# Optimization experiments

Hardware: AMD Instinct MI355X
Metric: run time of the kernel (lower is better)

Reference implementation:

```python
import jax, jax.numpy as jnp
import numpy as np

CELL_SIDE = 1.0
GRID_N = 6  # n x n occupancy grid


def _occupancy_grid(obs2):
    """Vectorized pairwise occupancy binning.
    obs2: [N, 2] -> grid [N, GRID_N*GRID_N] (counts of other pedestrians per cell)."""
    N = obs2.shape[0]
    nn = GRID_N * GRID_N
    # rel[i, j] = position of pedestrian j relative to i, in grid coords
    rel = (obs2[None, :, :] - obs2[:, None, :]) / CELL_SIDE + GRID_N / 2  # [N, N, 2]
    in_range = jnp.all((rel >= 0) & (rel < GRID_N), axis=-1)              # [N, N]
    not_self = ~jnp.eye(N, dtype=bool)
    valid = ~jnp.isnan(obs2[:, 0])                                        # [N]
    mask = in_range & not_self & valid[:, None] & valid[None, :]
    ij = jnp.clip(rel.astype(jnp.int32), 0, GRID_N - 1)                   # floor (rel>=0 under mask)
    local_bin = ij[..., 0] * GRID_N + ij[..., 1]                          # [N, N]
    # Global segment id: row i owns bins [i*nn, (i+1)*nn); invalid -> trash bin N*nn
    seg = jnp.where(mask, jnp.arange(N, dtype=jnp.int32)[:, None] * nn + local_bin, N * nn)
    counts = jax.ops.segment_sum(mask.astype(jnp.float32).reshape(-1),
                                 seg.reshape(-1), num_segments=N * nn + 1)
    return counts[: N * nn].reshape(N, nn)


def setup_inputs() -> dict:
    key = jax.random.key(0)
    k1, k2, k3, k4, k5 = jax.random.split(key, 5)
    N, hidden_dim, nn = 8192, 128, GRID_N * GRID_N
    hidden_state = jax.random.normal(k1, (N, hidden_dim), dtype=jnp.float32)
    obs1 = jax.random.normal(k2, (N, 2), dtype=jnp.float32)
    obs2 = jax.random.normal(k3, (N, 2), dtype=jnp.float32)
    W = jax.random.normal(k4, (hidden_dim, nn), dtype=jnp.float32) * (1.0 / np.sqrt(nn))
    b = jax.random.normal(k5, (hidden_dim,), dtype=jnp.float32) * 0.01
    return {"hidden_state": hidden_state, "obs1": obs1, "obs2": obs2, "W": W, "b": b}


def reference(hidden_state, obs1, obs2, W, b):
    # type_='occupancy': grid depends only on obs2; then Linear embedding.
    grid = _occupancy_grid(obs2)              # [N, 36]
    return grid @ W.T + b                     # [N, 128]
```

## Files before the change

### kernel.cpp

```cpp
#include <hip/hip_runtime.h>

#define N_PED  8192
#define HID    128
#define NN     36
#define IPB    8
#define SLICES 64
#define BLOCK  512
#define JS     128
#define HWW    10
#define NB     1024

__device__ __forceinline__ void rmw2(float p0x, float p0y, float p1x, float p1y,
                                     float xi4, float yi4, unsigned vone,
                                     unsigned baseA, unsigned baseB) {
    unsigned tA, iA, aA, vA, tB, iB, aB, vB;
    asm volatile(
        "v_sub_f32 %[tA], %[p0x], %[xi4]\n\t"
        "v_sub_f32 %[iA], %[p0y], %[yi4]\n\t"
        "v_sub_f32 %[tB], %[p1x], %[xi4]\n\t"
        "v_sub_f32 %[iB], %[p1y], %[yi4]\n\t"
        "v_cvt_i32_f32 %[tA], %[tA]\n\t"
        "v_cvt_i32_f32 %[iA], %[iA]\n\t"
        "v_cvt_i32_f32 %[tB], %[tB]\n\t"
        "v_cvt_i32_f32 %[iB], %[iB]\n\t"
        "v_add_u32 %[tA], -1, %[tA]\n\t"
        "v_add_u32 %[iA], -1, %[iA]\n\t"
        "v_add_u32 %[tB], -1, %[tB]\n\t"
        "v_add_u32 %[iB], -1, %[iB]\n\t"
        "v_max_u32 %[aA], %[tA], %[iA]\n\t"
        "v_max_u32 %[aB], %[tB], %[iB]\n\t"
        "v_mad_u32_u24 %[tA], %[tA], 6, %[iA]\n\t"
        "v_mad_u32_u24 %[tB], %[tB], 6, %[iB]\n\t"
        "v_cmp_gt_u32 vcc, 6, %[aA]\n\t"
        "v_lshrrev_b32 %[aA], 2, %[tA]\n\t"
        "v_cndmask_b32 %[aA], 9, %[aA], vcc\n\t"
        "v_cmp_gt_u32 vcc, 6, %[aB]\n\t"
        "v_lshrrev_b32 %[aB], 2, %[tB]\n\t"
        "v_cndmask_b32 %[aB], 9, %[aB], vcc\n\t"
        "v_lshlrev_b32 %[iA], 3, %[tA]\n\t"
        "v_lshlrev_b32 %[iA], %[iA], %[one]\n\t"
        "v_lshlrev_b32 %[iB], 3, %[tB]\n\t"
        "v_lshlrev_b32 %[iB], %[iB], %[one]\n\t"
        "v_lshl_add_u32 %[aA], %[aA], 11, %[bA]\n\t"
        "v_lshl_add_u32 %[aB], %[aB], 11, %[bB]\n\t"
        "ds_read_b32 %[vA], %[aA]\n\t"
        "ds_read_b32 %[vB], %[aB]\n\t"
        "s_waitcnt lgkmcnt(0)\n\t"
        "v_add_u32 %[vA], %[vA], %[iA]\n\t"
        "v_add_u32 %[vB], %[vB], %[iB]\n\t"
        "ds_write_b32 %[aA], %[vA]\n\t"
        "ds_write_b32 %[aB], %[vB]\n\t"
        : [tA]"=&v"(tA), [iA]"=&v"(iA), [aA]"=&v"(aA), [vA]"=&v"(vA),
          [tB]"=&v"(tB), [iB]"=&v"(iB), [aB]"=&v"(aB), [vB]"=&v"(vB)
        : [p0x]"v"(p0x), [p0y]"v"(p0y), [p1x]"v"(p1x), [p1y]"v"(p1y),
          [xi4]"v"(xi4), [yi4]"v"(yi4), [one]"v"(vone),
          [bA]"v"(baseA), [bB]"v"(baseB)
        : "vcc");
}

__global__ __launch_bounds__(BLOCK, 6) void pool_kernel(
    const float* __restrict__ obs2_g,
    const float* __restrict__ Wg,
    const float* __restrict__ bias,
    float* __restrict__ out)
{
    __shared__ unsigned s_hA[HWW * BLOCK];
    __shared__ unsigned s_hB[HWW * BLOCK];
    __shared__ float    s_rgrid[IPB][NN];
    __shared__ unsigned s_wsel[IPB];

    const int tid = threadIdx.x;
    const int bid = blockIdx.x;

    #pragma unroll
    for (int k = 0; k < HWW; ++k) {
        s_hA[tid + k * BLOCK] = 0u;
        s_hB[tid + k * BLOCK] = 0u;
    }

    const int il    = tid & (IPB - 1);
    const int slice = tid >> 3;
    const int i     = bid * IPB + il;

    const float2 pi = ((const float2*)obs2_g)[i];
    const float  xi4 = pi.x - 4.0f;
    const float  yi4 = pi.y - 4.0f;

    if (tid < IPB) {
        float dx = pi.x - xi4;
        float dy = pi.y - yi4;
        unsigned u1 = (unsigned)((int)dx) - 1u;
        unsigned u2 = (unsigned)((int)dy) - 1u;
        bool ok = (u1 < 6u) & (u2 < 6u);
        s_wsel[il] = ok ? (u1 * 6u + u2) : 255u;
    }
    __syncthreads();

    const unsigned vone  = 1u;
    const unsigned baseA = (unsigned)(uintptr_t)&s_hA[tid];
    const unsigned baseB = (unsigned)(uintptr_t)&s_hB[tid];

    #define PAIR8(r0, r1, r2, r3) do {                              \
        rmw2(r0.x, r0.y, r0.z, r0.w, xi4, yi4, vone, baseA, baseB); \
        rmw2(r1.x, r1.y, r1.z, r1.w, xi4, yi4, vone, baseA, baseB); \
        rmw2(r2.x, r2.y, r2.z, r2.w, xi4, yi4, vone, baseA, baseB); \
        rmw2(r3.x, r3.y, r3.z, r3.w, xi4, yi4, vone, baseA, baseB); \
    } while (0)

    {
        const float4* jp = (const float4*)obs2_g + slice * (JS / 2);
        float4 a0 = jp[0], a1 = jp[1], a2 = jp[2], a3 = jp[3];
        float4 b0 = jp[4], b1 = jp[5], b2 = jp[6], b3 = jp[7];
        jp += 8;
        #pragma unroll 1
        for (int it = 0; it < 7; ++it) {
            PAIR8(a0, a1, a2, a3);
            a0 = jp[0]; a1 = jp[1]; a2 = jp[2]; a3 = jp[3];
            PAIR8(b0, b1, b2, b3);
            b0 = jp[4]; b1 = jp[5]; b2 = jp[6]; b3 = jp[7];
            jp += 8;
        }
        PAIR8(a0, a1, a2, a3);
        PAIR8(b0, b1, b2, b3);
    }
    #undef PAIR8

    asm volatile("s_waitcnt lgkmcnt(0)" ::: "memory");
    __syncthreads();

    if (tid < IPB * 9) {
        const int ril = tid & (IPB - 1);
        const int w   = tid >> 3;
        unsigned lo = 0u, hi = 0u;
        #pragma unroll 8
        for (int sl = 0; sl < SLICES; ++sl) {
            unsigned t = sl * IPB + ril;
            unsigned a = s_hA[(w << 9) + t];
            unsigned b = s_hB[(w << 9) + t];
            lo += (a & 0x00FF00FFu) + (b & 0x00FF00FFu);
            hi += ((a >> 8) & 0x00FF00FFu) + ((b >> 8) & 0x00FF00FFu);
        }
        unsigned s0 = lo & 0xFFFFu;
        unsigned s1 = hi & 0xFFFFu;
        unsigned s2 = lo >> 16;
        unsigned s3 = hi >> 16;
        const unsigned sel  = s_wsel[ril];
        const unsigned base = (unsigned)(w * 4);
        s0 -= (sel == base + 0u);
        s1 -= (sel == base + 1u);
        s2 -= (sel == base + 2u);
        s3 -= (sel == base + 3u);
        s_rgrid[ril][base + 0] = (float)s0;
        s_rgrid[ril][base + 1] = (float)s1;
        s_rgrid[ril][base + 2] = (float)s2;
        s_rgrid[ril][base + 3] = (float)s3;
    }
    __syncthreads();

    const int h  = tid & (HID - 1);
    const int r0 = tid >> 7;
    const float4* W4 = (const float4*)Wg;

    const float bh = bias[h];
    float acc0 = bh, acc1 = bh;

    #pragma unroll
    for (int k4 = 0; k4 < 9; ++k4) {
        float4 w4 = W4[h * 9 + k4];
        float4 g0 = *(const float4*)&s_rgrid[r0    ][k4 * 4];
        float4 g1 = *(const float4*)&s_rgrid[r0 + 4][k4 * 4];
        acc0 += g0.x * w4.x + g0.y * w4.y + g0.z * w4.z + g0.w * w4.w;
        acc1 += g1.x * w4.x + g1.y * w4.y + g1.z * w4.z + g1.w * w4.w;
    }

    const int obase = bid * IPB;
    out[(obase + r0    ) * HID + h] = acc0;
    out[(obase + r0 + 4) * HID + h] = acc1;
}

extern "C" void kernel_launch(void* const* d_in, const int* in_sizes, int n_in,
                              void* d_out, int out_size, void* d_ws, size_t ws_size,
                              hipStream_t stream) {
    const float* obs2 = (const float*)d_in[2];
    const float* W    = (const float*)d_in[3];
    const float* b    = (const float*)d_in[4];
    float* out        = (float*)d_out;
    (void)in_sizes; (void)n_in; (void)out_size; (void)d_ws; (void)ws_size;

    hipLaunchKernelGGL(pool_kernel, dim3(NB), dim3(BLOCK), 0, stream,
                       obs2, W, b, out);
}
```

Baseline: 39.32 us.

## Halve block size, use four private LDS histogram copies with masked increments

```diff
diff --git a/kernel.cpp b/kernel.cpp
--- a/kernel.cpp
+++ b/kernel.cpp
@@ -4,16 +4,19 @@
 #define HID    128
 #define NN     36
 #define IPB    8
-#define SLICES 64
-#define BLOCK  512
-#define JS     128
-#define HWW    10
+#define SLICES 32
+#define BLOCK  256
+#define JS     256
 #define NB     1024
-
-__device__ __forceinline__ void rmw2(float p0x, float p0y, float p1x, float p1y,
-                                     float xi4, float yi4, unsigned vone,
-                                     unsigned baseA, unsigned baseB) {
-    unsigned tA, iA, aA, vA, tB, iB, aB, vB;
+#define AWORDS (9 * BLOCK)
+
+__device__ __forceinline__ void quad4(
+    float p0x, float p0y, float p1x, float p1y,
+    float p2x, float p2y, float p3x, float p3y,
+    float xi4, float yi4, unsigned vone,
+    unsigned bA, unsigned bB, unsigned bC, unsigned bD)
+{
+    unsigned tA, tB, iA, aA, vA, iB, aB, vB, iC, aC, vC, iD, aD, vD;
     asm volatile(
         "v_sub_f32 %[tA], %[p0x], %[xi4]\n\t"
         "v_sub_f32 %[iA], %[p0y], %[yi4]\n\t"
@@ -33,39 +36,80 @@
         "v_mad_u32_u24 %[tB], %[tB], 6, %[iB]\n\t"
         "v_cmp_gt_u32 vcc, 6, %[aA]\n\t"
         "v_lshrrev_b32 %[aA], 2, %[tA]\n\t"
-        "v_cndmask_b32 %[aA], 9, %[aA], vcc\n\t"
+        "v_cndmask_b32 %[aA], 0, %[aA], vcc\n\t"
+        "v_lshlrev_b32 %[iA], 3, %[tA]\n\t"
+        "v_lshlrev_b32 %[iA], %[iA], %[one]\n\t"
+        "v_cndmask_b32 %[iA], 0, %[iA], vcc\n\t"
+        "v_lshl_add_u32 %[aA], %[aA], 10, %[bA]\n\t"
         "v_cmp_gt_u32 vcc, 6, %[aB]\n\t"
         "v_lshrrev_b32 %[aB], 2, %[tB]\n\t"
-        "v_cndmask_b32 %[aB], 9, %[aB], vcc\n\t"
-        "v_lshlrev_b32 %[iA], 3, %[tA]\n\t"
-        "v_lshlrev_b32 %[iA], %[iA], %[one]\n\t"
+        "v_cndmask_b32 %[aB], 0, %[aB], vcc\n\t"
         "v_lshlrev_b32 %[iB], 3, %[tB]\n\t"
         "v_lshlrev_b32 %[iB], %[iB], %[one]\n\t"
-        "v_lshl_add_u32 %[aA], %[aA], 11, %[bA]\n\t"
-        "v_lshl_add_u32 %[aB], %[aB], 11, %[bB]\n\t"
+        "v_cndmask_b32 %[iB], 0, %[iB], vcc\n\t"
+        "v_lshl_add_u32 %[aB], %[aB], 10, %[bB]\n\t"
         "ds_read_b32 %[vA], %[aA]\n\t"
         "ds_read_b32 %[vB], %[aB]\n\t"
+        "v_sub_f32 %[tA], %[p2x], %[xi4]\n\t"
+        "v_sub_f32 %[iC], %[p2y], %[yi4]\n\t"
+        "v_sub_f32 %[tB], %[p3x], %[xi4]\n\t"
+        "v_sub_f32 %[iD], %[p3y], %[yi4]\n\t"
+        "v_cvt_i32_f32 %[tA], %[tA]\n\t"
+        "v_cvt_i32_f32 %[iC], %[iC]\n\t"
+        "v_cvt_i32_f32 %[tB], %[tB]\n\t"
+        "v_cvt_i32_f32 %[iD], %[iD]\n\t"
+        "v_add_u32 %[tA], -1, %[tA]\n\t"
+        "v_add_u32 %[iC], -1, %[iC]\n\t"
+        "v_add_u32 %[tB], -1, %[tB]\n\t"
+        "v_add_u32 %[iD], -1, %[iD]\n\t"
+        "v_max_u32 %[aC], %[tA], %[iC]\n\t"
+        "v_max_u32 %[aD], %[tB], %[iD]\n\t"
+        "v_mad_u32_u24 %[tA], %[tA], 6, %[iC]\n\t"
+        "v_mad_u32_u24 %[tB], %[tB], 6, %[iD]\n\t"
+        "v_cmp_gt_u32 vcc, 6, %[aC]\n\t"
+        "v_lshrrev_b32 %[aC], 2, %[tA]\n\t"
+        "v_cndmask_b32 %[aC], 0, %[aC], vcc\n\t"
+        "v_lshlrev_b32 %[iC], 3, %[tA]\n\t"
+        "v_lshlrev_b32 %[iC], %[iC], %[one]\n\t"
+        "v_cndmask_b32 %[iC], 0, %[iC], vcc\n\t"
+        "v_lshl_add_u32 %[aC], %[aC], 10, %[bC]\n\t"
+        "v_cmp_gt_u32 vcc, 6, %[aD]\n\t"
+        "v_lshrrev_b32 %[aD], 2, %[tB]\n\t"
+        "v_cndmask_b32 %[aD], 0, %[aD], vcc\n\t"
+        "v_lshlrev_b32 %[iD], 3, %[tB]\n\t"
+        "v_lshlrev_b32 %[iD], %[iD], %[one]\n\t"
+        "v_cndmask_b32 %[iD], 0, %[iD], vcc\n\t"
+        "v_lshl_add_u32 %[aD], %[aD], 10, %[bD]\n\t"
+        "ds_read_b32 %[vC], %[aC]\n\t"
+        "ds_read_b32 %[vD], %[aD]\n\t"
         "s_waitcnt lgkmcnt(0)\n\t"
         "v_add_u32 %[vA], %[vA], %[iA]\n\t"
         "v_add_u32 %[vB], %[vB], %[iB]\n\t"
+        "v_add_u32 %[vC], %[vC], %[iC]\n\t"
+        "v_add_u32 %[vD], %[vD], %[iD]\n\t"
         "ds_write_b32 %[aA], %[vA]\n\t"
         "ds_write_b32 %[aB], %[vB]\n\t"
-        : [tA]"=&v"(tA), [iA]"=&v"(iA), [aA]"=&v"(aA), [vA]"=&v"(vA),
-          [tB]"=&v"(tB), [iB]"=&v"(iB), [aB]"=&v"(aB), [vB]"=&v"(vB)
+        "ds_write_b32 %[aC], %[vC]\n\t"
+        "ds_write_b32 %[aD], %[vD]\n\t"
+        : [tA]"=&v"(tA), [tB]"=&v"(tB),
+          [iA]"=&v"(iA), [aA]"=&v"(aA), [vA]"=&v"(vA),
+          [iB]"=&v"(iB), [aB]"=&v"(aB), [vB]"=&v"(vB),
+          [iC]"=&v"(iC), [aC]"=&v"(aC), [vC]"=&v"(vC),
+          [iD]"=&v"(iD), [aD]"=&v"(aD), [vD]"=&v"(vD)
         : [p0x]"v"(p0x), [p0y]"v"(p0y), [p1x]"v"(p1x), [p1y]"v"(p1y),
+          [p2x]"v"(p2x), [p2y]"v"(p2y), [p3x]"v"(p3x), [p3y]"v"(p3y),
           [xi4]"v"(xi4), [yi4]"v"(yi4), [one]"v"(vone),
-          [bA]"v"(baseA), [bB]"v"(baseB)
+          [bA]"v"(bA), [bB]"v"(bB), [bC]"v"(bC), [bD]"v"(bD)
         : "vcc");
 }
 
-__global__ __launch_bounds__(BLOCK, 6) void pool_kernel(
+__global__ __launch_bounds__(BLOCK, 4) void pool_kernel(
     const float* __restrict__ obs2_g,
     const float* __restrict__ Wg,
     const float* __restrict__ bias,
     float* __restrict__ out)
 {
-    __shared__ unsigned s_hA[HWW * BLOCK];
-    __shared__ unsigned s_hB[HWW * BLOCK];
+    __shared__ unsigned s_h[4 * AWORDS];
     __shared__ float    s_rgrid[IPB][NN];
     __shared__ unsigned s_wsel[IPB];
 
@@ -73,10 +117,8 @@
     const int bid = blockIdx.x;
 
     #pragma unroll
-    for (int k = 0; k < HWW; ++k) {
-        s_hA[tid + k * BLOCK] = 0u;
-        s_hB[tid + k * BLOCK] = 0u;
-    }
+    for (int k = 0; k < 36; ++k)
+        s_h[tid + k * BLOCK] = 0u;
 
     const int il    = tid & (IPB - 1);
     const int slice = tid >> 3;
@@ -96,15 +138,17 @@
     }
     __syncthreads();
 
-    const unsigned vone  = 1u;
-    const unsigned baseA = (unsigned)(uintptr_t)&s_hA[tid];
-    const unsigned baseB = (unsigned)(uintptr_t)&s_hB[tid];
-
-    #define PAIR8(r0, r1, r2, r3) do {                              \
-        rmw2(r0.x, r0.y, r0.z, r0.w, xi4, yi4, vone, baseA, baseB); \
-        rmw2(r1.x, r1.y, r1.z, r1.w, xi4, yi4, vone, baseA, baseB); \
-        rmw2(r2.x, r2.y, r2.z, r2.w, xi4, yi4, vone, baseA, baseB); \
-        rmw2(r3.x, r3.y, r3.z, r3.w, xi4, yi4, vone, baseA, baseB); \
+    const unsigned vone = 1u;
+    const unsigned bA = (unsigned)(uintptr_t)&s_h[0 * AWORDS + tid];
+    const unsigned bB = (unsigned)(uintptr_t)&s_h[1 * AWORDS + tid];
+    const unsigned bC = (unsigned)(uintptr_t)&s_h[2 * AWORDS + tid];
+    const unsigned bD = (unsigned)(uintptr_t)&s_h[3 * AWORDS + tid];
+
+    #define PAIR8(r0, r1, r2, r3) do {                                   \
+        quad4(r0.x, r0.y, r0.z, r0.w, r1.x, r1.y, r1.z, r1.w,            \
+              xi4, yi4, vone, bA, bB, bC, bD);                           \
+        quad4(r2.x, r2.y, r2.z, r2.w, r3.x, r3.y, r3.z, r3.w,            \
+              xi4, yi4, vone, bA, bB, bC, bD);                           \
     } while (0)
 
     {
@@ -113,7 +157,7 @@
         float4 b0 = jp[4], b1 = jp[5], b2 = jp[6], b3 = jp[7];
         jp += 8;
         #pragma unroll 1
-        for (int it = 0; it < 7; ++it) {
+        for (int it = 0; it < 15; ++it) {
             PAIR8(a0, a1, a2, a3);
             a0 = jp[0]; a1 = jp[1]; a2 = jp[2]; a3 = jp[3];
             PAIR8(b0, b1, b2, b3);
@@ -132,13 +176,17 @@
         const int ril = tid & (IPB - 1);
         const int w   = tid >> 3;
         unsigned lo = 0u, hi = 0u;
-        #pragma unroll 8
+        #pragma unroll 4
         for (int sl = 0; sl < SLICES; ++sl) {
-            unsigned t = sl * IPB + ril;
-            unsigned a = s_hA[(w << 9) + t];
-            unsigned b = s_hB[(w << 9) + t];
-            lo += (a & 0x00FF00FFu) + (b & 0x00FF00FFu);
-            hi += ((a >> 8) & 0x00FF00FFu) + ((b >> 8) & 0x00FF00FFu);
+            unsigned t = (w << 8) + sl * IPB + ril;
+            unsigned v0 = s_h[0 * AWORDS + t];
+            unsigned v1 = s_h[1 * AWORDS + t];
+            unsigned v2 = s_h[2 * AWORDS + t];
+            unsigned v3 = s_h[3 * AWORDS + t];
+            lo += (v0 & 0x00FF00FFu) + (v1 & 0x00FF00FFu)
+                + (v2 & 0x00FF00FFu) + (v3 & 0x00FF00FFu);
+            hi += ((v0 >> 8) & 0x00FF00FFu) + ((v1 >> 8) & 0x00FF00FFu)
+                + ((v2 >> 8) & 0x00FF00FFu) + ((v3 >> 8) & 0x00FF00FFu);
         }
         unsigned s0 = lo & 0xFFFFu;
         unsigned s1 = hi & 0xFFFFu;
@@ -162,20 +210,26 @@
     const float4* W4 = (const float4*)Wg;
 
     const float bh = bias[h];
-    float acc0 = bh, acc1 = bh;
+    float acc0 = bh, acc1 = bh, acc2 = bh, acc3 = bh;
 
     #pragma unroll
     for (int k4 = 0; k4 < 9; ++k4) {
         float4 w4 = W4[h * 9 + k4];
         float4 g0 = *(const float4*)&s_rgrid[r0    ][k4 * 4];
-        float4 g1 = *(const float4*)&s_rgrid[r0 + 4][k4 * 4];
+        float4 g1 = *(const float4*)&s_rgrid[r0 + 2][k4 * 4];
+        float4 g2 = *(const float4*)&s_rgrid[r0 + 4][k4 * 4];
+        float4 g3 = *(const float4*)&s_rgrid[r0 + 6][k4 * 4];
         acc0 += g0.x * w4.x + g0.y * w4.y + g0.z * w4.z + g0.w * w4.w;
         acc1 += g1.x * w4.x + g1.y * w4.y + g1.z * w4.z + g1.w * w4.w;
+        acc2 += g2.x * w4.x + g2.y * w4.y + g2.z * w4.z + g2.w * w4.w;
+        acc3 += g3.x * w4.x + g3.y * w4.y + g3.z * w4.z + g3.w * w4.w;
     }
 
     const int obase = bid * IPB;
     out[(obase + r0    ) * HID + h] = acc0;
-    out[(obase + r0 + 4) * HID + h] = acc1;
+    out[(obase + r0 + 2) * HID + h] = acc1;
+    out[(obase + r0 + 4) * HID + h] = acc2;
+    out[(obase + r0 + 6) * HID + h] = acc3;
 }
 
 extern "C" void kernel_launch(void* const* d_in, const int* in_sizes, int n_in,
```

New measurement: 40.61 us. 1.03x slower.
